# Kernel optimization log

Hardware: AMD Instinct MI355X
Metric: run time of the kernel (lower is better)

Reference implementation:

```python
import jax, jax.numpy as jnp
import numpy as np
from functools import partial

DM, DP, DV = 128, 32, 32
DO = DP + DV
SCALE_F = 4.0
MAXF = 127.0 / SCALE_F                       # 31.75 feature clamp
SCALE_FM = SCALE_F / 16.0 * 3600.0 / 256.0   # scale after spatial mean
MAXM = 127.0 / SCALE_FM                      # clamp after mean
DN = ('NCHW', 'OIHW', 'NCHW')

# 3-tap positions inside a 3x3 kernel for the 4 directions
_DIR_POS = [
    [(1, 0), (1, 1), (1, 2)],  # horizontal
    [(0, 1), (1, 1), (2, 1)],  # vertical
    [(0, 0), (1, 1), (2, 2)],  # main diagonal
    [(2, 0), (1, 1), (0, 2)],  # anti diagonal
]

def _dir_conv(x, w, b, d):
    # w: [3, out, in] -> dense [out, in, 3, 3] kernel with 3 nonzero taps
    o, i = w.shape[1], w.shape[2]
    k = jnp.zeros((o, i, 3, 3), w.dtype)
    for t, (r, c) in enumerate(_DIR_POS[d]):
        k = k.at[:, :, r, c].set(w[t])
    y = jax.lax.conv_general_dilated(x, k, (1, 1), 'SAME', dimension_numbers=DN)
    return y + b[None, :, None, None]

def _pw(x, w, b):  # 1x1 conv: w [out, in]
    return jnp.einsum('bchw,oc->bohw', x, w) + b[None, :, None, None]

def _lrelu16(x):
    return jnp.where(x >= 0, x, x * (1.0 / 16.0))

def forward(x, map_w, map_b, dconv_w, dconv_b, c1_w, c1_b,
            r0_w1, r0_b1, r0_w2, r0_b2, fin_w, fin_b, prelu_w,
            pdw_w, pdw_b, ppw_w, vl1_w, vl1_b, vl2_w, vl2_b,
            vlf_w, vlf_b, pscale, vscale):
    silu = jax.nn.silu
    # ---- Mapping ----
    xs = tuple(silu(_dir_conv(x, map_w, map_b, d)) for d in range(4))
    for l in range(4):  # 4 DirectionalConvResBlocks
        res = xs
        xs = tuple(silu(_dir_conv(xs[d], dconv_w[l], dconv_b[l], d)) for d in range(4))
        xs = tuple(silu(_pw(t, c1_w[l], c1_b[l])) for t in xs)
        xs = tuple(a + b for a, b in zip(xs, res))
    # Conv0dResBlock
    res = xs
    xs = tuple(silu(_pw(t, r0_w1, r0_b1)) for t in xs)
    xs = tuple(silu(_pw(t, r0_w2, r0_b2)) for t in xs)
    xs = tuple(a + b for a, b in zip(xs, res))
    xs = tuple(_pw(t, fin_w, fin_b) for t in xs)
    feature = jnp.stack(xs, axis=1)  # [B, 4, DO, H, W]
    # ---- trunk post-processing ----
    feature = jnp.tanh(feature / MAXF) * MAXF
    feature = jnp.sum(feature, axis=1)  # [B, DO, H, W]
    a = prelu_w[None, :, None, None]
    feature = jnp.where(feature >= 0, feature, a * feature)  # PReLU per-channel
    feature = feature / 4.0
    # ---- policy head ----
    policy = feature[:, :DP]
    policy = jax.lax.conv_general_dilated(policy, pdw_w, (1, 1), 'SAME',
                                          dimension_numbers=DN,
                                          feature_group_count=DP)
    policy = _lrelu16(policy + pdw_b[None, :, None, None])
    policy = jnp.clip(policy, -MAXF, MAXF)
    policy = _lrelu16(jnp.einsum('bchw,oc->bohw', policy, ppw_w))
    policy = policy * pscale
    # ---- value head ----
    value = jnp.mean(feature[:, DP:], axis=(2, 3))  # [B, DV]
    value = jax.nn.relu(value)
    value = jax.nn.relu(value @ vl1_w.T + vl1_b)
    value = jnp.minimum(value, MAXM)
    value = jax.nn.relu(value @ vl2_w.T + vl2_b)
    value = jnp.minimum(value, MAXM)
    value = (value @ vlf_w.T + vlf_b) * vscale
    return (value, policy)

def setup_inputs() -> dict:
    key = jax.random.key(0)
    ks = iter(jax.random.split(key, 32))
    n = lambda shape, s=0.1: (jax.random.normal(next(ks), shape, jnp.float32) * s)
    B, H, W = 512, 15, 15
    return {
        'x': jax.random.uniform(next(ks), (B, 2, H, W), jnp.float32),
        'map_w': n((3, DM, 2), 0.5), 'map_b': jnp.zeros((DM,), jnp.float32),
        'dconv_w': n((4, 3, DM, DM)), 'dconv_b': jnp.zeros((4, DM), jnp.float32),
        'c1_w': n((4, DM, DM)), 'c1_b': jnp.zeros((4, DM), jnp.float32),
        'r0_w1': n((DM, DM)), 'r0_b1': jnp.zeros((DM,), jnp.float32),
        'r0_w2': n((DM, DM)), 'r0_b2': jnp.zeros((DM,), jnp.float32),
        'fin_w': n((DO, DM)), 'fin_b': jnp.zeros((DO,), jnp.float32),
        'prelu_w': jnp.full((DO,), 0.25, jnp.float32),
        'pdw_w': n((DP, 1, 3, 3), 0.3), 'pdw_b': jnp.zeros((DP,), jnp.float32),
        'ppw_w': n((1, DP), 0.3),
        'vl1_w': n((DV, DV), 0.2), 'vl1_b': jnp.zeros((DV,), jnp.float32),
        'vl2_w': n((DV, DV), 0.2), 'vl2_b': jnp.zeros((DV,), jnp.float32),
        'vlf_w': n((3, DV), 0.2), 'vlf_b': jnp.zeros((3,), jnp.float32),
        'pscale': jnp.ones((1,), jnp.float32),
        'vscale': jnp.ones((1,), jnp.float32),
    }

def reference(x, map_w, map_b, dconv_w, dconv_b, c1_w, c1_b,
              r0_w1, r0_b1, r0_w2, r0_b2, fin_w, fin_b, prelu_w,
              pdw_w, pdw_b, ppw_w, vl1_w, vl1_b, vl2_w, vl2_b,
              vlf_w, vlf_b, pscale, vscale):
    return forward(x, map_w, map_b, dconv_w, dconv_b, c1_w, c1_b,
                   r0_w1, r0_b1, r0_w2, r0_b2, fin_w, fin_b, prelu_w,
                   pdw_w, pdw_b, ppw_w, vl1_w, vl1_b, vl2_w, vl2_b,
                   vlf_w, vlf_b, pscale, vscale)
```

## Files before the change

kernel.cpp:

```cpp
#include <hip/hip_runtime.h>
#include <math.h>

typedef unsigned short u16;
typedef _Float16 f16;
typedef __attribute__((ext_vector_type(4))) _Float16 f16x4;
typedef __attribute__((ext_vector_type(8))) _Float16 f16x8;
typedef __attribute__((ext_vector_type(4))) float f32x4;

#define NCELL 225
#define AST   136
#define NROW  227
#define MAXF  31.75f
#define MAXM  (127.0f/((4.0f/16.0f)*3600.0f/256.0f))
#define DYN_LDS (2*NROW*AST*2)

#define W_DCONV 0
#define W_C1    196608
#define W_R01   262144
#define W_R02   278528
#define W_FIN   294912
#define W_F16TOT 303104
#define F_MAPB   0
#define F_DCONVB 128
#define F_C1B    640
#define F_R0B1   1152
#define F_R0B2   1280
#define F_FINB   1408
#define F_PRELU  1472
#define F_MAPW   1536
#define F_TOT    2304

__device__ __forceinline__ float bfu(unsigned h){ union{unsigned i; float f;} v; v.i=h<<16; return v.f; }
__device__ __forceinline__ float rcp_f(float x){ return __builtin_amdgcn_rcpf(x); }
__device__ __forceinline__ float silu_f(float x){ return x*rcp_f(1.f+__expf(-x)); }
__device__ __forceinline__ float tanh_f(float z){ return 1.f - 2.f*rcp_f(__expf(2.f*z)+1.f); }
__device__ __forceinline__ float ldp(const void* p, size_t i, int isf){
  return isf ? ((const float*)p)[i] : bfu(((const u16*)p)[i]);
}

__global__ __launch_bounds__(256) void k_prep(
    const void* __restrict__ dconv_w, const void* __restrict__ c1_w,
    const void* __restrict__ r0_w1,  const void* __restrict__ r0_w2,
    const void* __restrict__ fin_w,  const void* __restrict__ map_w,
    const void* __restrict__ map_b,  const void* __restrict__ dconv_b,
    const void* __restrict__ c1_b,   const void* __restrict__ r0_b1,
    const void* __restrict__ r0_b2,  const void* __restrict__ fin_b,
    const void* __restrict__ prelu_w,
    const void* __restrict__ x, f16* __restrict__ wbuf)
{
  __shared__ int sflag;
  if (threadIdx.x < 64) {
    unsigned v = ((const u16*)x)[2*threadIdx.x];
    unsigned long long m = __ballot(v > 0x4000u);
    if (threadIdx.x == 0) sflag = (__popcll(m) > 16) ? 1 : 0;
  }
  __syncthreads();
  const int isf = sflag;
  float* fsec = (float*)(wbuf + W_F16TOT);
  const int NTOT = W_F16TOT + F_TOT;
  for (int i = blockIdx.x*256 + threadIdx.x; i < NTOT; i += gridDim.x*256) {
    if (i < W_F16TOT) {
      float v; int j = i;
      if (j < 196608)                 v = ldp(dconv_w, j, isf);
      else if ((j -= 196608) < 65536) v = ldp(c1_w, j, isf);
      else if ((j -= 65536) < 16384)  v = ldp(r0_w1, j, isf);
      else if ((j -= 16384) < 16384)  v = ldp(r0_w2, j, isf);
      else { j -= 16384;              v = ldp(fin_w, j, isf); }
      wbuf[i] = (f16)v;
    } else {
      int j = i - W_F16TOT; float v;
      if (j < 128)               v = ldp(map_b, j, isf);
      else if ((j -= 128) < 512) v = ldp(dconv_b, j, isf);
      else if ((j -= 512) < 512) v = ldp(c1_b, j, isf);
      else if ((j -= 512) < 128) v = ldp(r0_b1, j, isf);
      else if ((j -= 128) < 128) v = ldp(r0_b2, j, isf);
      else if ((j -= 128) < 64)  v = ldp(fin_b, j, isf);
      else if ((j -= 64) < 64)   v = ldp(prelu_w, j, isf);
      else { j -= 64;            v = ldp(map_w, j, isf); }
      fsec[i - W_F16TOT] = v;
    }
  }
}

template<int NTAPS, int MODE>
__device__ __forceinline__ void phase(
    const f16* __restrict__ S, f16* __restrict__ D,
    const f16* __restrict__ W, const float* __restrict__ bp,
    const int (&aoffB)[4][3], const int (&stoff)[4],
    int ch0, int wrow)
{
  f32x4 acc[4][2];
#pragma unroll
  for (int mi = 0; mi < 4; ++mi) {
    f32x4 z = {0.f,0.f,0.f,0.f};
    acc[mi][0] = z; acc[mi][1] = z;
  }
#pragma unroll
  for (int t = 0; t < NTAPS; ++t) {
    const int tt = (NTAPS == 3) ? t : 1;
    const f16* Wt = W + ((NTAPS == 3) ? t*16384 : 0) + wrow;
#pragma clang loop unroll(disable)
    for (int kb = 0; kb < 4; ++kb) {
      f16x8 Wf0 = *(const f16x8*)(Wt + kb*32);
      f16x8 Wf1 = *(const f16x8*)(Wt + 2048 + kb*32);
      f16x8 Af[4];
#pragma unroll
      for (int mi = 0; mi < 4; ++mi)
        Af[mi] = *(const f16x8*)((const char*)S + aoffB[mi][tt] + kb*64);
#pragma unroll
      for (int mi = 0; mi < 4; ++mi) {
        acc[mi][0] = __builtin_amdgcn_mfma_f32_16x16x32_f16(Wf0, Af[mi], acc[mi][0], 0, 0, 0);
        acc[mi][1] = __builtin_amdgcn_mfma_f32_16x16x32_f16(Wf1, Af[mi], acc[mi][1], 0, 0, 0);
      }
    }
  }
  f32x4 bb0 = *(const f32x4*)(bp + ch0);
  f32x4 bb1 = *(const f32x4*)(bp + ch0 + 16);
#pragma unroll
  for (int mi = 0; mi < 4; ++mi)
#pragma unroll
    for (int nt = 0; nt < 2; ++nt) {
      f16* dp = D + stoff[mi] + ch0 + nt*16;
      const f32x4 bb = nt ? bb1 : bb0;
      float v0 = silu_f(acc[mi][nt][0] + bb[0]);
      float v1 = silu_f(acc[mi][nt][1] + bb[1]);
      float v2 = silu_f(acc[mi][nt][2] + bb[2]);
      float v3 = silu_f(acc[mi][nt][3] + bb[3]);
      if (MODE == 1) {
        f16x4 r = *(const f16x4*)dp;
        v0 += (float)r[0]; v1 += (float)r[1]; v2 += (float)r[2]; v3 += (float)r[3];
      }
      f16x4 o = { (f16)v0, (f16)v1, (f16)v2, (f16)v3 };
      *(f16x4*)dp = o;
    }
  __syncthreads();
}

__global__ __launch_bounds__(1024, 4) void k_all(
    const void* __restrict__ x,
    const void* __restrict__ pdw_w,  const void* __restrict__ pdw_b,
    const void* __restrict__ ppw_w,
    const void* __restrict__ vl1_w,  const void* __restrict__ vl1_b,
    const void* __restrict__ vl2_w,  const void* __restrict__ vl2_b,
    const void* __restrict__ vlf_w,  const void* __restrict__ vlf_b,
    const void* __restrict__ pscale, const void* __restrict__ vscale,
    const f16* __restrict__ wbuf, float* __restrict__ out, int badflag)
{
  extern __shared__ __align__(16) char dyn[];
  f16* bufA = (f16*)dyn;
  f16* bufB = bufA + NROW*AST;
  __shared__ float xin[452];
  __shared__ float vred[1024];
  __shared__ float vvA[32], vvB[32];
  __shared__ int sflag;

  const int b = blockIdx.x, tid = threadIdx.x;
  const int lane = tid & 63, wave = tid >> 6;
  const int cg = wave >> 2, ng = wave & 3;
  const int quad = lane >> 4, lrow = lane & 15;
  const int ch0 = ng*32 + quad*4;
  const int wrow = (ng*32 + lrow)*128 + quad*8;
  const float* fsec = (const float*)(wbuf + W_F16TOT);

  if (tid < 64) {
    unsigned v = ((const u16*)x)[2*tid];
    unsigned long long m = __ballot(v > 0x4000u);
    if (tid == 0) sflag = (__popcll(m) > 16) ? 1 : 0;
  }
  for (int i = tid; i < AST; i += 1024) {
    bufA[225*AST + i] = (f16)0.f;
    bufB[225*AST + i] = (f16)0.f;
  }
  __syncthreads();
  const int isf = sflag;

  for (int i = tid; i < 452; i += 1024) {
    float v;
    if (i < 225)       v = ldp(x, (size_t)b*450 + i, isf);
    else if (i == 225) v = 0.f;
    else if (i < 451)  v = ldp(x, (size_t)b*450 + 225 + (i - 226), isf);
    else               v = 0.f;
    xin[i] = v;
  }

  int cellv[4], stoff[4], fcl[4], rr4[4], cc4[4];
#pragma unroll
  for (int mi = 0; mi < 4; ++mi) {
    const int cell = (cg*4 + mi)*16 + lrow;
    cellv[mi] = cell;
    rr4[mi] = cell / 15;
    cc4[mi] = cell - rr4[mi]*15;
    stoff[mi] = ((cell < NCELL) ? cell : 226) * AST;
    fcl[mi]   = (cell < NCELL) ? cell : 225;
  }

  float facc[4][4];
#pragma unroll
  for (int mi = 0; mi < 4; ++mi)
#pragma unroll
    for (int j = 0; j < 4; ++j) facc[mi][j] = 0.f;

  const int DRt[4] = {0, 1, 1, -1};
  const int DCt[4] = {1, 0, 1, 1};

  __syncthreads();

#pragma clang loop unroll(disable)
  for (int d = 0; d < 4; ++d) {
    const int dr = DRt[d], dc = DCt[d];

    int pcell[4][3];
#pragma unroll
    for (int mi = 0; mi < 4; ++mi) {
      const bool v0 = cellv[mi] < NCELL;
#pragma unroll
      for (int t = 0; t < 3; ++t) {
        const int rs = rr4[mi] + (t-1)*dr, cs = cc4[mi] + (t-1)*dc;
        const bool v = v0 & (rs >= 0) & (rs < 15) & (cs >= 0) & (cs < 15);
        pcell[mi][t] = v ? rs*15 + cs : 225;
      }
    }

    {
      f32x4 w[2][3][2], mb[2];
#pragma unroll
      for (int nt = 0; nt < 2; ++nt) {
        const int chn = ch0 + nt*16;
        mb[nt] = *(const f32x4*)(fsec + F_MAPB + chn);
#pragma unroll
        for (int t = 0; t < 3; ++t) {
          w[nt][t][0] = *(const f32x4*)(fsec + F_MAPW + (t*128 + chn)*2);
          w[nt][t][1] = *(const f32x4*)(fsec + F_MAPW + (t*128 + chn)*2 + 4);
        }
      }
#pragma unroll
      for (int mi = 0; mi < 4; ++mi) {
        float x0[3], x1[3];
#pragma unroll
        for (int t = 0; t < 3; ++t) {
          const int sp = pcell[mi][t];
          x0[t] = xin[sp]; x1[t] = xin[226 + sp];
        }
#pragma unroll
        for (int nt = 0; nt < 2; ++nt) {
          f16x4 o;
#pragma unroll
          for (int j = 0; j < 4; ++j) {
            float s = mb[nt][j];
#pragma unroll
            for (int t = 0; t < 3; ++t)
              s += w[nt][t][j>>1][(j&1)*2]*x0[t] + w[nt][t][j>>1][(j&1)*2+1]*x1[t];
            o[j] = (f16)silu_f(s);
          }
          *(f16x4*)(bufA + stoff[mi] + ch0 + nt*16) = o;
        }
      }
    }
    __syncthreads();

    int aoffB[4][3];
#pragma unroll
    for (int mi = 0; mi < 4; ++mi)
#pragma unroll
      for (int t = 0; t < 3; ++t)
        aoffB[mi][t] = pcell[mi][t]*(AST*2) + quad*16;

#pragma clang loop unroll(disable)
    for (int l = 0; l < 4; ++l) {
      phase<3, 0>(bufA, bufB, wbuf + W_DCONV + (size_t)l*49152,
                  fsec + F_DCONVB + l*128, aoffB, stoff, ch0, wrow);
      phase<1, 1>(bufB, bufA, wbuf + W_C1 + (size_t)l*16384,
                  fsec + F_C1B + l*128, aoffB, stoff, ch0, wrow);
    }
    phase<1, 0>(bufA, bufB, wbuf + W_R01, fsec + F_R0B1, aoffB, stoff, ch0, wrow);
    phase<1, 1>(bufB, bufA, wbuf + W_R02, fsec + F_R0B2, aoffB, stoff, ch0, wrow);

    {
      f32x4 fa[4];
#pragma unroll
      for (int mi = 0; mi < 4; ++mi) { f32x4 z = {0.f,0.f,0.f,0.f}; fa[mi] = z; }
      const f16* Wt = wbuf + W_FIN + (ng*16 + lrow)*128 + quad*8;
#pragma clang loop unroll(disable)
      for (int kb = 0; kb < 4; ++kb) {
        f16x8 Wf = *(const f16x8*)(Wt + kb*32);
#pragma unroll
        for (int mi = 0; mi < 4; ++mi) {
          f16x8 a = *(const f16x8*)((const char*)bufA + aoffB[mi][1] + kb*64);
          fa[mi] = __builtin_amdgcn_mfma_f32_16x16x32_f16(Wf, a, fa[mi], 0, 0, 0);
        }
      }
      const int chf = ng*16 + quad*4;
      f32x4 fb = *(const f32x4*)(fsec + F_FINB + chf);
#pragma unroll
      for (int mi = 0; mi < 4; ++mi)
#pragma unroll
        for (int j = 0; j < 4; ++j)
          facc[mi][j] += tanh_f((fa[mi][j] + fb[j]) * (1.f/MAXF)) * MAXF;
    }
    __syncthreads();
  }

  float* featf = (float*)bufA;
  {
    const int chf = ng*16 + quad*4;
    f32x4 aw = *(const f32x4*)(fsec + F_PRELU + chf);
#pragma unroll
    for (int mi = 0; mi < 4; ++mi) {
      f32x4 o;
#pragma unroll
      for (int j = 0; j < 4; ++j) {
        float s = facc[mi][j];
        s = (s >= 0.f) ? s : aw[j]*s;
        o[j] = s * 0.25f;
      }
      *(f32x4*)(featf + fcl[mi]*64 + chf) = o;
    }
  }
  __syncthreads();

  {
    const int ch = tid >> 5, strip = tid & 31;
    float s = 0.f;
    for (int cell = strip; cell < NCELL; cell += 32)
      s += featf[cell*64 + 32 + ch];
    vred[tid] = s;
  }
  __syncthreads();
  if (tid < 32) {
    float s = 0.f;
#pragma unroll
    for (int k = 0; k < 32; ++k) s += vred[tid*32 + k];
    vvA[tid] = fmaxf(s * (1.f/225.f), 0.f);
  }
  __syncthreads();
  if (tid < 32) {
    float s = ldp(vl1_b, tid, isf);
    for (int c2 = 0; c2 < 32; ++c2) s += ldp(vl1_w, tid*32 + c2, isf) * vvA[c2];
    vvB[tid] = fminf(fmaxf(s, 0.f), MAXM);
  }
  __syncthreads();
  if (tid < 32) {
    float s = ldp(vl2_b, tid, isf);
    for (int c2 = 0; c2 < 32; ++c2) s += ldp(vl2_w, tid*32 + c2, isf) * vvB[c2];
    vvA[tid] = fminf(fmaxf(s, 0.f), MAXM);
  }
  __syncthreads();
  if (tid < 3) {
    float s = ldp(vlf_b, tid, isf);
    for (int c2 = 0; c2 < 32; ++c2) s += ldp(vlf_w, tid*32 + c2, isf) * vvA[c2];
    out[b*3 + tid] = s * ldp(vscale, 0, isf);
  }
  __syncthreads();

  for (int i = tid; i < NCELL*32; i += 1024) {
    const int cell = i >> 5, ch = i & 31;
    const int r = cell/15, c = cell - r*15;
    float s = ldp(pdw_b, ch, isf);
#pragma unroll
    for (int kr = 0; kr < 3; ++kr)
#pragma unroll
      for (int kc = 0; kc < 3; ++kc) {
        const int rr = r + kr - 1, cc = c + kc - 1;
        if (rr >= 0 && rr < 15 && cc >= 0 && cc < 15)
          s += ldp(pdw_w, (size_t)ch*9 + kr*3 + kc, isf) * featf[(rr*15 + cc)*64 + ch];
      }
    s = (s >= 0.f) ? s : s * (1.f/16.f);
    s = fminf(fmaxf(s, -MAXF), MAXF);
    featf[cell*64 + 32 + ch] = s;
  }
  __syncthreads();

  const float psc = ldp(pscale, 0, isf);
  for (int cell = tid; cell < NCELL; cell += 1024) {
    float s = 0.f;
#pragma unroll
    for (int c2 = 0; c2 < 32; ++c2)
      s += ldp(ppw_w, c2, isf) * featf[cell*64 + 32 + c2];
    s = (s >= 0.f) ? s : s * (1.f/16.f);
    out[1536 + b*NCELL + cell] = s * psc;
  }

  if (badflag && b == 0 && tid == 0) out[0] = 100000.f;
}

extern "C" void kernel_launch(void* const* d_in, const int* in_sizes, int n_in,
                              void* d_out, int out_size, void* d_ws, size_t ws_size,
                              hipStream_t stream)
{
  static const int EXP[25] = {230400, 768, 128, 196608, 512, 65536, 512,
                              16384, 128, 16384, 128, 8192, 64, 64,
                              288, 32, 32, 1024, 32, 1024, 32, 96, 3, 1, 1};
  int bad = (n_in != 25) ? 1 : 0;
  if (!bad) for (int i = 0; i < 25; ++i) if (in_sizes[i] != EXP[i]) bad = 1;
  if (out_size != 116736) bad = 1;

  if (hipFuncSetAttribute(reinterpret_cast<const void*>(k_all),
                          hipFuncAttributeMaxDynamicSharedMemorySize,
                          DYN_LDS) != hipSuccess) bad = 1;

  f16* wbuf = (f16*)d_ws;

  k_prep<<<512, 256, 0, stream>>>(d_in[3], d_in[5], d_in[7], d_in[9], d_in[11],
                                  d_in[1], d_in[2], d_in[4], d_in[6], d_in[8],
                                  d_in[10], d_in[12], d_in[13], d_in[0], wbuf);

  k_all<<<512, 1024, DYN_LDS, stream>>>(
      d_in[0], d_in[14], d_in[15], d_in[16],
      d_in[17], d_in[18], d_in[19], d_in[20], d_in[21], d_in[22],
      d_in[23], d_in[24], wbuf, (float*)d_out, bad);
}
```

Before: 993.4 us.

## Retile MFMA waves to 2 cell tiles by 64 channels and hoist depthwise weights

Changes the per-wave tile from 4 cell-tiles × 32 output channels to 2 cell-tiles × 64 output channels. Each A fragment read from LDS now feeds four MFMAs instead of two, which cuts LDS reads of activations; weight fragment loads from global/L2 double per wave. The kb loops are unrolled, and the mapping, final projection and PReLU stages are remapped to the new layout. The depthwise-conv weights and bias are now loaded once per thread instead of inside the inner loop.

```diff
diff --git a/kernel.cpp b/kernel.cpp
--- a/kernel.cpp
+++ b/kernel.cpp
@@ -86,46 +86,50 @@
 __device__ __forceinline__ void phase(
     const f16* __restrict__ S, f16* __restrict__ D,
     const f16* __restrict__ W, const float* __restrict__ bp,
-    const int (&aoffB)[4][3], const int (&stoff)[4],
+    const int (&aoffB)[2][3], const int (&stoff)[2],
     int ch0, int wrow)
 {
-  f32x4 acc[4][2];
-#pragma unroll
-  for (int mi = 0; mi < 4; ++mi) {
-    f32x4 z = {0.f,0.f,0.f,0.f};
-    acc[mi][0] = z; acc[mi][1] = z;
-  }
+  f32x4 acc[2][4];
+#pragma unroll
+  for (int mi = 0; mi < 2; ++mi)
+#pragma unroll
+    for (int nt = 0; nt < 4; ++nt) { f32x4 z = {0.f,0.f,0.f,0.f}; acc[mi][nt] = z; }
+
 #pragma unroll
   for (int t = 0; t < NTAPS; ++t) {
     const int tt = (NTAPS == 3) ? t : 1;
     const f16* Wt = W + ((NTAPS == 3) ? t*16384 : 0) + wrow;
-#pragma clang loop unroll(disable)
+#pragma unroll
     for (int kb = 0; kb < 4; ++kb) {
       f16x8 Wf0 = *(const f16x8*)(Wt + kb*32);
       f16x8 Wf1 = *(const f16x8*)(Wt + 2048 + kb*32);
-      f16x8 Af[4];
-#pragma unroll
-      for (int mi = 0; mi < 4; ++mi)
-        Af[mi] = *(const f16x8*)((const char*)S + aoffB[mi][tt] + kb*64);
-#pragma unroll
-      for (int mi = 0; mi < 4; ++mi) {
-        acc[mi][0] = __builtin_amdgcn_mfma_f32_16x16x32_f16(Wf0, Af[mi], acc[mi][0], 0, 0, 0);
-        acc[mi][1] = __builtin_amdgcn_mfma_f32_16x16x32_f16(Wf1, Af[mi], acc[mi][1], 0, 0, 0);
-      }
-    }
-  }
-  f32x4 bb0 = *(const f32x4*)(bp + ch0);
-  f32x4 bb1 = *(const f32x4*)(bp + ch0 + 16);
-#pragma unroll
-  for (int mi = 0; mi < 4; ++mi)
-#pragma unroll
-    for (int nt = 0; nt < 2; ++nt) {
+      f16x8 Wf2 = *(const f16x8*)(Wt + 4096 + kb*32);
+      f16x8 Wf3 = *(const f16x8*)(Wt + 6144 + kb*32);
+      f16x8 A0 = *(const f16x8*)((const char*)S + aoffB[0][tt] + kb*64);
+      f16x8 A1 = *(const f16x8*)((const char*)S + aoffB[1][tt] + kb*64);
+      acc[0][0] = __builtin_amdgcn_mfma_f32_16x16x32_f16(Wf0, A0, acc[0][0], 0, 0, 0);
+      acc[1][0] = __builtin_amdgcn_mfma_f32_16x16x32_f16(Wf0, A1, acc[1][0], 0, 0, 0);
+      acc[0][1] = __builtin_amdgcn_mfma_f32_16x16x32_f16(Wf1, A0, acc[0][1], 0, 0, 0);
+      acc[1][1] = __builtin_amdgcn_mfma_f32_16x16x32_f16(Wf1, A1, acc[1][1], 0, 0, 0);
+      acc[0][2] = __builtin_amdgcn_mfma_f32_16x16x32_f16(Wf2, A0, acc[0][2], 0, 0, 0);
+      acc[1][2] = __builtin_amdgcn_mfma_f32_16x16x32_f16(Wf2, A1, acc[1][2], 0, 0, 0);
+      acc[0][3] = __builtin_amdgcn_mfma_f32_16x16x32_f16(Wf3, A0, acc[0][3], 0, 0, 0);
+      acc[1][3] = __builtin_amdgcn_mfma_f32_16x16x32_f16(Wf3, A1, acc[1][3], 0, 0, 0);
+    }
+  }
+
+  f32x4 bb[4];
+#pragma unroll
+  for (int nt = 0; nt < 4; ++nt) bb[nt] = *(const f32x4*)(bp + ch0 + nt*16);
+#pragma unroll
+  for (int mi = 0; mi < 2; ++mi)
+#pragma unroll
+    for (int nt = 0; nt < 4; ++nt) {
       f16* dp = D + stoff[mi] + ch0 + nt*16;
-      const f32x4 bb = nt ? bb1 : bb0;
-      float v0 = silu_f(acc[mi][nt][0] + bb[0]);
-      float v1 = silu_f(acc[mi][nt][1] + bb[1]);
-      float v2 = silu_f(acc[mi][nt][2] + bb[2]);
-      float v3 = silu_f(acc[mi][nt][3] + bb[3]);
+      float v0 = silu_f(acc[mi][nt][0] + bb[nt][0]);
+      float v1 = silu_f(acc[mi][nt][1] + bb[nt][1]);
+      float v2 = silu_f(acc[mi][nt][2] + bb[nt][2]);
+      float v3 = silu_f(acc[mi][nt][3] + bb[nt][3]);
       if (MODE == 1) {
         f16x4 r = *(const f16x4*)dp;
         v0 += (float)r[0]; v1 += (float)r[1]; v2 += (float)r[2]; v3 += (float)r[3];
@@ -156,10 +160,10 @@
 
   const int b = blockIdx.x, tid = threadIdx.x;
   const int lane = tid & 63, wave = tid >> 6;
-  const int cg = wave >> 2, ng = wave & 3;
+  const int cg = wave >> 1, ng = wave & 1;
   const int quad = lane >> 4, lrow = lane & 15;
-  const int ch0 = ng*32 + quad*4;
-  const int wrow = (ng*32 + lrow)*128 + quad*8;
+  const int ch0 = ng*64 + quad*4;
+  const int wrow = (ng*64 + lrow)*128 + quad*8;
   const float* fsec = (const float*)(wbuf + W_F16TOT);
 
   if (tid < 64) {
@@ -183,10 +187,10 @@
     xin[i] = v;
   }
 
-  int cellv[4], stoff[4], fcl[4], rr4[4], cc4[4];
-#pragma unroll
-  for (int mi = 0; mi < 4; ++mi) {
-    const int cell = (cg*4 + mi)*16 + lrow;
+  int cellv[2], stoff[2], fcl[2], rr4[2], cc4[2];
+#pragma unroll
+  for (int mi = 0; mi < 2; ++mi) {
+    const int cell = (cg*2 + mi)*16 + lrow;
     cellv[mi] = cell;
     rr4[mi] = cell / 15;
     cc4[mi] = cell - rr4[mi]*15;
@@ -194,24 +198,22 @@
     fcl[mi]   = (cell < NCELL) ? cell : 225;
   }
 
-  float facc[4][4];
-#pragma unroll
-  for (int mi = 0; mi < 4; ++mi)
-#pragma unroll
-    for (int j = 0; j < 4; ++j) facc[mi][j] = 0.f;
-
-  const int DRt[4] = {0, 1, 1, -1};
-  const int DCt[4] = {1, 0, 1, 1};
+  f32x4 facc[2][2];
+  {
+    f32x4 z = {0.f,0.f,0.f,0.f};
+    facc[0][0] = z; facc[0][1] = z; facc[1][0] = z; facc[1][1] = z;
+  }
 
   __syncthreads();
 
 #pragma clang loop unroll(disable)
   for (int d = 0; d < 4; ++d) {
-    const int dr = DRt[d], dc = DCt[d];
-
-    int pcell[4][3];
-#pragma unroll
-    for (int mi = 0; mi < 4; ++mi) {
+    const int dr = (d == 0) ? 0 : ((d == 3) ? -1 : 1);
+    const int dc = (d == 1) ? 0 : 1;
+
+    int pcell[2][3];
+#pragma unroll
+    for (int mi = 0; mi < 2; ++mi) {
       const bool v0 = cellv[mi] < NCELL;
 #pragma unroll
       for (int t = 0; t < 3; ++t) {
@@ -222,45 +224,44 @@
     }
 
     {
-      f32x4 w[2][3][2], mb[2];
-#pragma unroll
-      for (int nt = 0; nt < 2; ++nt) {
+      float x0[2][3], x1[2][3];
+#pragma unroll
+      for (int mi = 0; mi < 2; ++mi)
+#pragma unroll
+        for (int t = 0; t < 3; ++t) {
+          const int sp = pcell[mi][t];
+          x0[mi][t] = xin[sp]; x1[mi][t] = xin[226 + sp];
+        }
+#pragma unroll
+      for (int nt = 0; nt < 4; ++nt) {
         const int chn = ch0 + nt*16;
-        mb[nt] = *(const f32x4*)(fsec + F_MAPB + chn);
+        f32x4 mb = *(const f32x4*)(fsec + F_MAPB + chn);
+        f32x4 wt[3][2];
 #pragma unroll
         for (int t = 0; t < 3; ++t) {
-          w[nt][t][0] = *(const f32x4*)(fsec + F_MAPW + (t*128 + chn)*2);
-          w[nt][t][1] = *(const f32x4*)(fsec + F_MAPW + (t*128 + chn)*2 + 4);
+          wt[t][0] = *(const f32x4*)(fsec + F_MAPW + (t*128 + chn)*2);
+          wt[t][1] = *(const f32x4*)(fsec + F_MAPW + (t*128 + chn)*2 + 4);
+        }
+#pragma unroll
+        for (int mi = 0; mi < 2; ++mi) {
+          f16x4 o;
+#pragma unroll
+          for (int j = 0; j < 4; ++j) {
+            float s = mb[j];
+#pragma unroll
+            for (int t = 0; t < 3; ++t)
+              s += wt[t][j>>1][(j&1)*2]*x0[mi][t] + wt[t][j>>1][(j&1)*2+1]*x1[mi][t];
+            o[j] = (f16)silu_f(s);
+          }
+          *(f16x4*)(bufA + stoff[mi] + chn) = o;
         }
       }
-#pragma unroll
-      for (int mi = 0; mi < 4; ++mi) {
-        float x0[3], x1[3];
-#pragma unroll
-        for (int t = 0; t < 3; ++t) {
-          const int sp = pcell[mi][t];
-          x0[t] = xin[sp]; x1[t] = xin[226 + sp];
-        }
-#pragma unroll
-        for (int nt = 0; nt < 2; ++nt) {
-          f16x4 o;
-#pragma unroll
-          for (int j = 0; j < 4; ++j) {
-            float s = mb[nt][j];
-#pragma unroll
-            for (int t = 0; t < 3; ++t)
-              s += w[nt][t][j>>1][(j&1)*2]*x0[t] + w[nt][t][j>>1][(j&1)*2+1]*x1[t];
-            o[j] = (f16)silu_f(s);
-          }
-          *(f16x4*)(bufA + stoff[mi] + ch0 + nt*16) = o;
-        }
-      }
     }
     __syncthreads();
 
-    int aoffB[4][3];
-#pragma unroll
-    for (int mi = 0; mi < 4; ++mi)
+    int aoffB[2][3];
+#pragma unroll
+    for (int mi = 0; mi < 2; ++mi)
 #pragma unroll
       for (int t = 0; t < 3; ++t)
         aoffB[mi][t] = pcell[mi][t]*(AST*2) + quad*16;
@@ -276,44 +277,53 @@
     phase<1, 1>(bufB, bufA, wbuf + W_R02, fsec + F_R0B2, aoffB, stoff, ch0, wrow);
 
     {
-      f32x4 fa[4];
-#pragma unroll
-      for (int mi = 0; mi < 4; ++mi) { f32x4 z = {0.f,0.f,0.f,0.f}; fa[mi] = z; }
-      const f16* Wt = wbuf + W_FIN + (ng*16 + lrow)*128 + quad*8;
-#pragma clang loop unroll(disable)
+      f32x4 fa[2][2];
+      { f32x4 z = {0.f,0.f,0.f,0.f}; fa[0][0]=z; fa[0][1]=z; fa[1][0]=z; fa[1][1]=z; }
+      const f16* Wt = wbuf + W_FIN + (ng*32 + lrow)*128 + quad*8;
+#pragma unroll
       for (int kb = 0; kb < 4; ++kb) {
-        f16x8 Wf = *(const f16x8*)(Wt + kb*32);
-#pragma unroll
-        for (int mi = 0; mi < 4; ++mi) {
-          f16x8 a = *(const f16x8*)((const char*)bufA + aoffB[mi][1] + kb*64);
-          fa[mi] = __builtin_amdgcn_mfma_f32_16x16x32_f16(Wf, a, fa[mi], 0, 0, 0);
+        f16x8 Wf0 = *(const f16x8*)(Wt + kb*32);
+        f16x8 Wf1 = *(const f16x8*)(Wt + 2048 + kb*32);
+        f16x8 A0 = *(const f16x8*)((const char*)bufA + aoffB[0][1] + kb*64);
+        f16x8 A1 = *(const f16x8*)((const char*)bufA + aoffB[1][1] + kb*64);
+        fa[0][0] = __builtin_amdgcn_mfma_f32_16x16x32_f16(Wf0, A0, fa[0][0], 0, 0, 0);
+        fa[1][0] = __builtin_amdgcn_mfma_f32_16x16x32_f16(Wf0, A1, fa[1][0], 0, 0, 0);
+        fa[0][1] = __builtin_amdgcn_mfma_f32_16x16x32_f16(Wf1, A0, fa[0][1], 0, 0, 0);
+        fa[1][1] = __builtin_amdgcn_mfma_f32_16x16x32_f16(Wf1, A1, fa[1][1], 0, 0, 0);
+      }
+      const int chf = ng*32 + quad*4;
+      f32x4 fb0 = *(const f32x4*)(fsec + F_FINB + chf);
+      f32x4 fb1 = *(const f32x4*)(fsec + F_FINB + chf + 16);
+#pragma unroll
+      for (int mi = 0; mi < 2; ++mi)
+#pragma unroll
+        for (int j = 0; j < 4; ++j) {
+          facc[mi][0][j] += tanh_f((fa[mi][0][j] + fb0[j]) * (1.f/MAXF)) * MAXF;
+          facc[mi][1][j] += tanh_f((fa[mi][1][j] + fb1[j]) * (1.f/MAXF)) * MAXF;
         }
-      }
-      const int chf = ng*16 + quad*4;
-      f32x4 fb = *(const f32x4*)(fsec + F_FINB + chf);
-#pragma unroll
-      for (int mi = 0; mi < 4; ++mi)
-#pragma unroll
-        for (int j = 0; j < 4; ++j)
-          facc[mi][j] += tanh_f((fa[mi][j] + fb[j]) * (1.f/MAXF)) * MAXF;
     }
     __syncthreads();
   }
 
   float* featf = (float*)bufA;
   {
-    const int chf = ng*16 + quad*4;
-    f32x4 aw = *(const f32x4*)(fsec + F_PRELU + chf);
-#pragma unroll
-    for (int mi = 0; mi < 4; ++mi) {
-      f32x4 o;
+    const int chf = ng*32 + quad*4;
+    f32x4 aw0 = *(const f32x4*)(fsec + F_PRELU + chf);
+    f32x4 aw1 = *(const f32x4*)(fsec + F_PRELU + chf + 16);
+#pragma unroll
+    for (int mi = 0; mi < 2; ++mi) {
+      f32x4 o0, o1;
 #pragma unroll
       for (int j = 0; j < 4; ++j) {
-        float s = facc[mi][j];
-        s = (s >= 0.f) ? s : aw[j]*s;
-        o[j] = s * 0.25f;
+        float s0 = facc[mi][0][j];
+        s0 = (s0 >= 0.f) ? s0 : aw0[j]*s0;
+        o0[j] = s0 * 0.25f;
+        float s1 = facc[mi][1][j];
+        s1 = (s1 >= 0.f) ? s1 : aw1[j]*s1;
+        o1[j] = s1 * 0.25f;
       }
-      *(f32x4*)(featf + fcl[mi]*64 + chf) = o;
+      *(f32x4*)(featf + fcl[mi]*64 + chf) = o0;
+      *(f32x4*)(featf + fcl[mi]*64 + chf + 16) = o1;
     }
   }
   __syncthreads();
@@ -352,21 +362,28 @@
   }
   __syncthreads();
 
-  for (int i = tid; i < NCELL*32; i += 1024) {
-    const int cell = i >> 5, ch = i & 31;
-    const int r = cell/15, c = cell - r*15;
-    float s = ldp(pdw_b, ch, isf);
-#pragma unroll
-    for (int kr = 0; kr < 3; ++kr)
-#pragma unroll
-      for (int kc = 0; kc < 3; ++kc) {
-        const int rr = r + kr - 1, cc = c + kc - 1;
-        if (rr >= 0 && rr < 15 && cc >= 0 && cc < 15)
-          s += ldp(pdw_w, (size_t)ch*9 + kr*3 + kc, isf) * featf[(rr*15 + cc)*64 + ch];
-      }
-    s = (s >= 0.f) ? s : s * (1.f/16.f);
-    s = fminf(fmaxf(s, -MAXF), MAXF);
-    featf[cell*64 + 32 + ch] = s;
+  {
+    const int ch = tid & 31;
+    float pw[9];
+#pragma unroll
+    for (int k = 0; k < 9; ++k) pw[k] = ldp(pdw_w, (size_t)ch*9 + k, isf);
+    const float pb = ldp(pdw_b, ch, isf);
+    for (int i = tid; i < NCELL*32; i += 1024) {
+      const int cell = i >> 5;
+      const int r = cell/15, c = cell - r*15;
+      float s = pb;
+#pragma unroll
+      for (int kr = 0; kr < 3; ++kr)
+#pragma unroll
+        for (int kc = 0; kc < 3; ++kc) {
+          const int rr = r + kr - 1, cc = c + kc - 1;
+          if (rr >= 0 && rr < 15 && cc >= 0 && cc < 15)
+            s += pw[kr*3 + kc] * featf[(rr*15 + cc)*64 + ch];
+        }
+      s = (s >= 0.f) ? s : s * (1.f/16.f);
+      s = fminf(fmaxf(s, -MAXF), MAXF);
+      featf[cell*64 + 32 + ch] = s;
+    }
   }
   __syncthreads();
 
```

New measurement: 1.780 ms. 79.2% more time.

## Use a single in-place LDS activation buffer and raise occupancy bound

Applied to the files above, without the earlier changes.

Replaces the ping-pong pair of LDS activation buffers with one buffer updated in place. Each phase adds a barrier between its MFMA reads and its epilogue writes, and the residual values are held in registers instead of being re-read from the destination. This halves dynamic LDS use and sets the launch bound to 8 waves per SIMD, aiming for more resident blocks per CU. Smaller edits reorder the mapping loop to cut live registers and hoist the depthwise-conv weights into registers. The costs are an extra barrier per phase and a tighter register budget, which may cause spills.

```diff
diff --git a/kernel.cpp b/kernel.cpp
--- a/kernel.cpp
+++ b/kernel.cpp
@@ -12,7 +12,7 @@
 #define NROW  227
 #define MAXF  31.75f
 #define MAXM  (127.0f/((4.0f/16.0f)*3600.0f/256.0f))
-#define DYN_LDS (2*NROW*AST*2)
+#define DYN_LDS (NROW*AST*2)
 
 #define W_DCONV 0
 #define W_C1    196608
@@ -84,10 +84,10 @@
 
 template<int NTAPS, int MODE>
 __device__ __forceinline__ void phase(
-    const f16* __restrict__ S, f16* __restrict__ D,
+    f16* __restrict__ buf,
     const f16* __restrict__ W, const float* __restrict__ bp,
     const int (&aoffB)[4][3], const int (&stoff)[4],
-    int ch0, int wrow)
+    int ch0, int wrow, const f16x4 (&res)[4][2])
 {
   f32x4 acc[4][2];
 #pragma unroll
@@ -106,7 +106,7 @@
       f16x8 Af[4];
 #pragma unroll
       for (int mi = 0; mi < 4; ++mi)
-        Af[mi] = *(const f16x8*)((const char*)S + aoffB[mi][tt] + kb*64);
+        Af[mi] = *(const f16x8*)((const char*)buf + aoffB[mi][tt] + kb*64);
 #pragma unroll
       for (int mi = 0; mi < 4; ++mi) {
         acc[mi][0] = __builtin_amdgcn_mfma_f32_16x16x32_f16(Wf0, Af[mi], acc[mi][0], 0, 0, 0);
@@ -116,19 +116,20 @@
   }
   f32x4 bb0 = *(const f32x4*)(bp + ch0);
   f32x4 bb1 = *(const f32x4*)(bp + ch0 + 16);
+  __syncthreads();
 #pragma unroll
   for (int mi = 0; mi < 4; ++mi)
 #pragma unroll
     for (int nt = 0; nt < 2; ++nt) {
-      f16* dp = D + stoff[mi] + ch0 + nt*16;
+      f16* dp = buf + stoff[mi] + ch0 + nt*16;
       const f32x4 bb = nt ? bb1 : bb0;
       float v0 = silu_f(acc[mi][nt][0] + bb[0]);
       float v1 = silu_f(acc[mi][nt][1] + bb[1]);
       float v2 = silu_f(acc[mi][nt][2] + bb[2]);
       float v3 = silu_f(acc[mi][nt][3] + bb[3]);
       if (MODE == 1) {
-        f16x4 r = *(const f16x4*)dp;
-        v0 += (float)r[0]; v1 += (float)r[1]; v2 += (float)r[2]; v3 += (float)r[3];
+        v0 += (float)res[mi][nt][0]; v1 += (float)res[mi][nt][1];
+        v2 += (float)res[mi][nt][2]; v3 += (float)res[mi][nt][3];
       }
       f16x4 o = { (f16)v0, (f16)v1, (f16)v2, (f16)v3 };
       *(f16x4*)dp = o;
@@ -136,7 +137,17 @@
   __syncthreads();
 }
 
-__global__ __launch_bounds__(1024, 4) void k_all(
+__device__ __forceinline__ void load_res(
+    const f16* __restrict__ buf, const int (&stoff)[4], int ch0, f16x4 (&res)[4][2])
+{
+#pragma unroll
+  for (int mi = 0; mi < 4; ++mi)
+#pragma unroll
+    for (int nt = 0; nt < 2; ++nt)
+      res[mi][nt] = *(const f16x4*)(buf + stoff[mi] + ch0 + nt*16);
+}
+
+__global__ __launch_bounds__(1024, 8) void k_all(
     const void* __restrict__ x,
     const void* __restrict__ pdw_w,  const void* __restrict__ pdw_b,
     const void* __restrict__ ppw_w,
@@ -147,8 +158,7 @@
     const f16* __restrict__ wbuf, float* __restrict__ out, int badflag)
 {
   extern __shared__ __align__(16) char dyn[];
-  f16* bufA = (f16*)dyn;
-  f16* bufB = bufA + NROW*AST;
+  f16* buf = (f16*)dyn;
   __shared__ float xin[452];
   __shared__ float vred[1024];
   __shared__ float vvA[32], vvB[32];
@@ -167,10 +177,8 @@
     unsigned long long m = __ballot(v > 0x4000u);
     if (tid == 0) sflag = (__popcll(m) > 16) ? 1 : 0;
   }
-  for (int i = tid; i < AST; i += 1024) {
-    bufA[225*AST + i] = (f16)0.f;
-    bufB[225*AST + i] = (f16)0.f;
-  }
+  for (int i = tid; i < AST; i += 1024)
+    buf[225*AST + i] = (f16)0.f;
   __syncthreads();
   const int isf = sflag;
 
@@ -194,20 +202,18 @@
     fcl[mi]   = (cell < NCELL) ? cell : 225;
   }
 
-  float facc[4][4];
+  float facc[4][2][2];
 #pragma unroll
   for (int mi = 0; mi < 4; ++mi)
 #pragma unroll
-    for (int j = 0; j < 4; ++j) facc[mi][j] = 0.f;
-
-  const int DRt[4] = {0, 1, 1, -1};
-  const int DCt[4] = {1, 0, 1, 1};
+    for (int jp = 0; jp < 2; ++jp) { facc[mi][jp][0] = 0.f; facc[mi][jp][1] = 0.f; }
 
   __syncthreads();
 
 #pragma clang loop unroll(disable)
   for (int d = 0; d < 4; ++d) {
-    const int dr = DRt[d], dc = DCt[d];
+    const int dr = (d == 0) ? 0 : ((d == 3) ? -1 : 1);
+    const int dc = (d == 1) ? 0 : 1;
 
     int pcell[4][3];
 #pragma unroll
@@ -222,37 +228,36 @@
     }
 
     {
-      f32x4 w[2][3][2], mb[2];
+      float x0[4][3], x1[4][3];
+#pragma unroll
+      for (int mi = 0; mi < 4; ++mi)
+#pragma unroll
+        for (int t = 0; t < 3; ++t) {
+          const int sp = pcell[mi][t];
+          x0[mi][t] = xin[sp]; x1[mi][t] = xin[226 + sp];
+        }
 #pragma unroll
       for (int nt = 0; nt < 2; ++nt) {
         const int chn = ch0 + nt*16;
-        mb[nt] = *(const f32x4*)(fsec + F_MAPB + chn);
+        f32x4 mb = *(const f32x4*)(fsec + F_MAPB + chn);
+        f32x4 wt[3][2];
 #pragma unroll
         for (int t = 0; t < 3; ++t) {
-          w[nt][t][0] = *(const f32x4*)(fsec + F_MAPW + (t*128 + chn)*2);
-          w[nt][t][1] = *(const f32x4*)(fsec + F_MAPW + (t*128 + chn)*2 + 4);
+          wt[t][0] = *(const f32x4*)(fsec + F_MAPW + (t*128 + chn)*2);
+          wt[t][1] = *(const f32x4*)(fsec + F_MAPW + (t*128 + chn)*2 + 4);
         }
-      }
-#pragma unroll
-      for (int mi = 0; mi < 4; ++mi) {
-        float x0[3], x1[3];
-#pragma unroll
-        for (int t = 0; t < 3; ++t) {
-          const int sp = pcell[mi][t];
-          x0[t] = xin[sp]; x1[t] = xin[226 + sp];
-        }
-#pragma unroll
-        for (int nt = 0; nt < 2; ++nt) {
+#pragma unroll
+        for (int mi = 0; mi < 4; ++mi) {
           f16x4 o;
 #pragma unroll
           for (int j = 0; j < 4; ++j) {
-            float s = mb[nt][j];
+            float s = mb[j];
 #pragma unroll
             for (int t = 0; t < 3; ++t)
-              s += w[nt][t][j>>1][(j&1)*2]*x0[t] + w[nt][t][j>>1][(j&1)*2+1]*x1[t];
+              s += wt[t][j>>1][(j&1)*2]*x0[mi][t] + wt[t][j>>1][(j&1)*2+1]*x1[mi][t];
             o[j] = (f16)silu_f(s);
           }
-          *(f16x4*)(bufA + stoff[mi] + ch0 + nt*16) = o;
+          *(f16x4*)(buf + stoff[mi] + chn) = o;
         }
       }
     }
@@ -265,15 +270,18 @@
       for (int t = 0; t < 3; ++t)
         aoffB[mi][t] = pcell[mi][t]*(AST*2) + quad*16;
 
+    f16x4 res[4][2];
 #pragma clang loop unroll(disable)
     for (int l = 0; l < 4; ++l) {
-      phase<3, 0>(bufA, bufB, wbuf + W_DCONV + (size_t)l*49152,
-                  fsec + F_DCONVB + l*128, aoffB, stoff, ch0, wrow);
-      phase<1, 1>(bufB, bufA, wbuf + W_C1 + (size_t)l*16384,
-                  fsec + F_C1B + l*128, aoffB, stoff, ch0, wrow);
-    }
-    phase<1, 0>(bufA, bufB, wbuf + W_R01, fsec + F_R0B1, aoffB, stoff, ch0, wrow);
-    phase<1, 1>(bufB, bufA, wbuf + W_R02, fsec + F_R0B2, aoffB, stoff, ch0, wrow);
+      load_res(buf, stoff, ch0, res);
+      phase<3, 0>(buf, wbuf + W_DCONV + (size_t)l*49152,
+                  fsec + F_DCONVB + l*128, aoffB, stoff, ch0, wrow, res);
+      phase<1, 1>(buf, wbuf + W_C1 + (size_t)l*16384,
+                  fsec + F_C1B + l*128, aoffB, stoff, ch0, wrow, res);
+    }
+    load_res(buf, stoff, ch0, res);
+    phase<1, 0>(buf, wbuf + W_R01, fsec + F_R0B1, aoffB, stoff, ch0, wrow, res);
+    phase<1, 1>(buf, wbuf + W_R02, fsec + F_R0B2, aoffB, stoff, ch0, wrow, res);
 
     {
       f32x4 fa[4];
@@ -285,7 +293,7 @@
         f16x8 Wf = *(const f16x8*)(Wt + kb*32);
 #pragma unroll
         for (int mi = 0; mi < 4; ++mi) {
-          f16x8 a = *(const f16x8*)((const char*)bufA + aoffB[mi][1] + kb*64);
+          f16x8 a = *(const f16x8*)((const char*)buf + aoffB[mi][1] + kb*64);
           fa[mi] = __builtin_amdgcn_mfma_f32_16x16x32_f16(Wf, a, fa[mi], 0, 0, 0);
         }
       }
@@ -295,12 +303,12 @@
       for (int mi = 0; mi < 4; ++mi)
 #pragma unroll
         for (int j = 0; j < 4; ++j)
-          facc[mi][j] += tanh_f((fa[mi][j] + fb[j]) * (1.f/MAXF)) * MAXF;
+          facc[mi][j>>1][j&1] += tanh_f((fa[mi][j] + fb[j]) * (1.f/MAXF)) * MAXF;
     }
     __syncthreads();
   }
 
-  float* featf = (float*)bufA;
+  float* featf = (float*)buf;
   {
     const int chf = ng*16 + quad*4;
     f32x4 aw = *(const f32x4*)(fsec + F_PRELU + chf);
@@ -309,7 +317,7 @@
       f32x4 o;
 #pragma unroll
       for (int j = 0; j < 4; ++j) {
-        float s = facc[mi][j];
+        float s = facc[mi][j>>1][j&1];
         s = (s >= 0.f) ? s : aw[j]*s;
         o[j] = s * 0.25f;
       }
@@ -352,21 +360,28 @@
   }
   __syncthreads();
 
-  for (int i = tid; i < NCELL*32; i += 1024) {
-    const int cell = i >> 5, ch = i & 31;
-    const int r = cell/15, c = cell - r*15;
-    float s = ldp(pdw_b, ch, isf);
-#pragma unroll
-    for (int kr = 0; kr < 3; ++kr)
-#pragma unroll
-      for (int kc = 0; kc < 3; ++kc) {
-        const int rr = r + kr - 1, cc = c + kc - 1;
-        if (rr >= 0 && rr < 15 && cc >= 0 && cc < 15)
-          s += ldp(pdw_w, (size_t)ch*9 + kr*3 + kc, isf) * featf[(rr*15 + cc)*64 + ch];
-      }
-    s = (s >= 0.f) ? s : s * (1.f/16.f);
-    s = fminf(fmaxf(s, -MAXF), MAXF);
-    featf[cell*64 + 32 + ch] = s;
+  {
+    const int ch = tid & 31;
+    float pw[9];
+#pragma unroll
+    for (int k = 0; k < 9; ++k) pw[k] = ldp(pdw_w, (size_t)ch*9 + k, isf);
+    const float pb = ldp(pdw_b, ch, isf);
+    for (int i = tid; i < NCELL*32; i += 1024) {
+      const int cell = i >> 5;
+      const int r = cell/15, c = cell - r*15;
+      float s = pb;
+#pragma unroll
+      for (int kr = 0; kr < 3; ++kr)
+#pragma unroll
+        for (int kc = 0; kc < 3; ++kc) {
+          const int rr = r + kr - 1, cc = c + kc - 1;
+          if (rr >= 0 && rr < 15 && cc >= 0 && cc < 15)
+            s += pw[kr*3 + kc] * featf[(rr*15 + cc)*64 + ch];
+        }
+      s = (s >= 0.f) ? s : s * (1.f/16.f);
+      s = fminf(fmaxf(s, -MAXF), MAXF);
+      featf[cell*64 + 32 + ch] = s;
+    }
   }
   __syncthreads();
 
```

Result: slower. 1.298 ms (+30.6%).
